# Optimization experiments

Hardware: AMD Instinct MI355X
Metric: run time of the kernel (lower is better)

The kernel has to match this reference:

```python
import jax, jax.numpy as jnp
import numpy as np

DIM = 2048
N_HEADS = 16
Q_LORA = 1536
KV_LORA = 512
NOPE = 128
ROPE = 64
QK_D = NOPE + ROPE  # 192
V_D = 128
EPS = 1e-6
B, S = 2, 2048


def rmsnorm(x, w, eps=EPS):
    return x * jax.lax.rsqrt(jnp.mean(x * x, axis=-1, keepdims=True) + eps) * w


def rotate_pe(x, cos, sin):
    # x: [B, S, H, ROPE]; cos/sin: [S, ROPE] -> broadcast [1, S, 1, ROPE]
    c = cos[None, :, None, :]
    s = sin[None, :, None, :]
    x1, x2 = jnp.split(x, 2, axis=-1)
    rot = jnp.concatenate([-x2, x1], axis=-1)
    return x * c + rot * s


def setup_inputs() -> dict:
    key = jax.random.key(0)
    ks = jax.random.split(key, 8)
    std = 0.02
    x = jax.random.normal(ks[0], (B, S, DIM), dtype=jnp.float32)
    # proper rotary tables
    inv_freq = 1.0 / (10000.0 ** (np.arange(0, ROPE, 2, dtype=np.float32) / ROPE))
    t = np.arange(S, dtype=np.float32)
    freqs = np.outer(t, inv_freq)  # [S, ROPE/2]
    emb = np.concatenate([freqs, freqs], axis=-1)  # [S, ROPE]
    cos = jnp.asarray(np.cos(emb))
    sin = jnp.asarray(np.sin(emb))
    wq_a = jax.random.normal(ks[1], (Q_LORA, DIM), dtype=jnp.float32) * std
    q_norm_w = jnp.ones((Q_LORA,), dtype=jnp.float32)
    wq_b = jax.random.normal(ks[2], (N_HEADS * QK_D, Q_LORA), dtype=jnp.float32) * std
    wkv_a = jax.random.normal(ks[3], (KV_LORA + ROPE, DIM), dtype=jnp.float32) * std
    kv_norm_w = jnp.ones((KV_LORA,), dtype=jnp.float32)
    wkv_b = jax.random.normal(ks[4], (N_HEADS * (NOPE + V_D), KV_LORA), dtype=jnp.float32) * std
    wo = jax.random.normal(ks[5], (DIM, N_HEADS * V_D), dtype=jnp.float32) * std
    return {"x": x, "cos": cos, "sin": sin, "wq_a": wq_a, "q_norm_w": q_norm_w,
            "wq_b": wq_b, "wkv_a": wkv_a, "kv_norm_w": kv_norm_w, "wkv_b": wkv_b, "wo": wo}


def mla_forward(x, cos, sin, wq_a, q_norm_w, wq_b, wkv_a, kv_norm_w, wkv_b, wo):
    bsz, seqlen, _ = x.shape
    scale = QK_D ** (-0.5)
    # Q path: low-rank down-proj -> RMSNorm -> up-proj
    q = rmsnorm(x @ wq_a.T, q_norm_w) @ wq_b.T
    q = q.reshape(bsz, seqlen, N_HEADS, QK_D)
    q_nope, q_pe = q[..., :NOPE], q[..., NOPE:]
    q_pe = rotate_pe(q_pe, cos, sin)
    q = jnp.concatenate([q_nope, q_pe], axis=-1)
    # KV path: shared low-rank latent + single rope slice
    kv = x @ wkv_a.T  # [B, S, KV_LORA + ROPE]
    kv_c, k_pe = kv[..., :KV_LORA], kv[..., KV_LORA:]
    k_pe = rotate_pe(k_pe[:, :, None, :], cos, sin)  # [B, S, 1, ROPE]
    kvb = rmsnorm(kv_c, kv_norm_w) @ wkv_b.T
    kvb = kvb.reshape(bsz, seqlen, N_HEADS, NOPE + V_D)
    k_nope, v = kvb[..., :NOPE], kvb[..., NOPE:]
    k = jnp.concatenate([k_nope, jnp.broadcast_to(k_pe, (bsz, seqlen, N_HEADS, ROPE))], axis=-1)
    # causal attention
    scores = jnp.einsum('bqhd,bkhd->bhqk', q, k) * scale
    mask = jnp.tril(jnp.ones((seqlen, seqlen), dtype=bool))
    scores = jnp.where(mask[None, None], scores, jnp.finfo(scores.dtype).min)
    p = jax.nn.softmax(scores, axis=-1)
    out = jnp.einsum('bhqk,bkhd->bqhd', p, v)
    out = out.reshape(bsz, seqlen, N_HEADS * V_D)
    return out @ wo.T


def reference(x, cos, sin, wq_a, q_norm_w, wq_b, wkv_a, kv_norm_w, wkv_b, wo):
    return mla_forward(x, cos, sin, wq_a, q_norm_w, wq_b, wkv_a, kv_norm_w, wkv_b, wo)
```

## Files before the change

### kernel.cpp

```cpp
#include <hip/hip_runtime.h>

typedef unsigned short u16;
typedef __attribute__((ext_vector_type(8))) short short8;
typedef __attribute__((ext_vector_type(4))) float floatx4;

__device__ __forceinline__ float bf2f(u16 u) {
  union { unsigned int i; float f; } v; v.i = ((unsigned int)u) << 16; return v.f;
}
__device__ __forceinline__ u16 f2bf(float f) {
  union { float f; unsigned int i; } v; v.f = f;
  unsigned int u = v.i;
  u += 0x7fffu + ((u >> 16) & 1u);
  return (u16)(u >> 16);
}

__device__ __forceinline__ void gld_lds16(const void* g, void* l) {
  __builtin_amdgcn_global_load_lds(
      (const __attribute__((address_space(1))) unsigned int*)g,
      (__attribute__((address_space(3))) unsigned int*)l, 16, 0, 0);
}

__global__ __launch_bounds__(256) void f2b_k(const float* __restrict__ s,
                                             u16* __restrict__ d, long n) {
  long i = ((long)blockIdx.x * 256 + threadIdx.x) * 4;
  if (i + 3 < n) {
    float4 v = *(const float4*)(s + i);
    d[i + 0] = f2bf(v.x); d[i + 1] = f2bf(v.y);
    d[i + 2] = f2bf(v.z); d[i + 3] = f2bf(v.w);
  } else {
    for (; i < n; i++) d[i] = f2bf(s[i]);
  }
}

__global__ __launch_bounds__(256) void wcat_k(const float* __restrict__ s1, int r1,
                                              const float* __restrict__ s2, int r2,
                                              u16* __restrict__ d, int cols, int rows_dst) {
  long i = (long)blockIdx.x * 256 + threadIdx.x;
  long total = (long)rows_dst * cols;
  if (i < total) {
    long r = i / cols, c = i - r * cols;
    float v = 0.f;
    if (r < r1) v = s1[r * cols + c];
    else if (r < r1 + r2) v = s2[(r - r1) * cols + c];
    d[i] = f2bf(v);
  }
}

template <int OUT_F32>
__global__ __launch_bounds__(256) void gemm_bt_mfma(
    const u16* __restrict__ A, int lda,
    const u16* __restrict__ W, int ldw,
    void* __restrict__ Cv, int ldc, int K) {
  __shared__ u16 Asm[128 * 32];
  __shared__ u16 Bsm[128 * 32];
  int tid = threadIdx.x;
  int lane = tid & 63, w = tid >> 6;
  int wm = (w >> 1) * 64, wn = (w & 1) * 64;
  int bm = blockIdx.y * 128, bn = blockIdx.x * 128;

  floatx4 acc[4][4];
#pragma unroll
  for (int i = 0; i < 4; i++)
#pragma unroll
    for (int j = 0; j < 4; j++) acc[i][j] = (floatx4){0.f, 0.f, 0.f, 0.f};

  int sr = lane >> 2;
  int sc = (lane & 3) * 8;
  int fr = lane & 15;
  int fq = (lane >> 4) * 8;

  for (int k0 = 0; k0 < K; k0 += 32) {
#pragma unroll
    for (int c = 0; c < 2; c++) {
      int row = 32 * w + 16 * c + sr;
      gld_lds16(A + (size_t)(bm + row) * lda + k0 + sc, &Asm[(32 * w + 16 * c) * 32]);
      gld_lds16(W + (size_t)(bn + row) * ldw + k0 + sc, &Bsm[(32 * w + 16 * c) * 32]);
    }
    __syncthreads();
    short8 af[4], bfr[4];
#pragma unroll
    for (int i = 0; i < 4; i++)
      af[i] = *(const short8*)&Asm[(wm + i * 16 + fr) * 32 + fq];
#pragma unroll
    for (int j = 0; j < 4; j++)
      bfr[j] = *(const short8*)&Bsm[(wn + j * 16 + fr) * 32 + fq];
#pragma unroll
    for (int i = 0; i < 4; i++)
#pragma unroll
      for (int j = 0; j < 4; j++)
        acc[i][j] = __builtin_amdgcn_mfma_f32_16x16x32_bf16(af[i], bfr[j], acc[i][j], 0, 0, 0);
    __syncthreads();
  }

  int cr = (lane >> 4) * 4, cc = lane & 15;
#pragma unroll
  for (int i = 0; i < 4; i++)
#pragma unroll
    for (int j = 0; j < 4; j++) {
      int col = bn + wn + j * 16 + cc;
#pragma unroll
      for (int r = 0; r < 4; r++) {
        size_t row = (size_t)(bm + wm + i * 16 + cr + r);
        if (OUT_F32) ((float*)Cv)[row * ldc + col] = acc[i][j][r];
        else         ((u16*)Cv)[row * ldc + col] = f2bf(acc[i][j][r]);
      }
    }
}

__global__ __launch_bounds__(256) void rmsnorm_k(
    const u16* __restrict__ in, const float* __restrict__ w,
    u16* __restrict__ out, int width, int stride) {
  int row = blockIdx.x;
  const u16* p = in + (size_t)row * stride;
  u16* o = out + (size_t)row * stride;
  float ss = 0.f;
  for (int i = threadIdx.x; i < width; i += 256) { float v = bf2f(p[i]); ss += v * v; }
  for (int off = 32; off > 0; off >>= 1) ss += __shfl_down(ss, off);
  __shared__ float red[4];
  if ((threadIdx.x & 63) == 0) red[threadIdx.x >> 6] = ss;
  __syncthreads();
  float inv = rsqrtf((red[0] + red[1] + red[2] + red[3]) / (float)width + 1e-6f);
  for (int i = threadIdx.x; i < width; i += 256)
    o[i] = f2bf(bf2f(p[i]) * inv * w[i]);
}

__global__ void rope_k(u16* __restrict__ base, int row_stride, int head_stride,
                       int head_off, const float* __restrict__ cosb,
                       const float* __restrict__ sinb, int S) {
  int t = blockIdx.x, h = blockIdx.y, i = threadIdx.x;
  int pos = t % S;
  u16* p = base + (size_t)t * row_stride + h * head_stride + head_off;
  float c1 = cosb[pos * 64 + i];
  float c2 = cosb[pos * 64 + i + 32];
  float s1 = sinb[pos * 64 + i];
  float s2 = sinb[pos * 64 + i + 32];
  float x1 = bf2f(p[i]), x2 = bf2f(p[i + 32]);
  p[i]      = f2bf(x1 * c1 - x2 * s1);
  p[i + 32] = f2bf(x2 * c2 + x1 * s2);
}

__global__ __launch_bounds__(256) void vtrans_k(
    const u16* __restrict__ kvb, u16* __restrict__ vt, int S) {
  int tb = blockIdx.x, h = blockIdx.y, b = blockIdx.z;
  __shared__ __align__(16) u16 Ts[64][136];
  int tid = threadIdx.x;
#pragma unroll
  for (int it = 0; it < 4; it++) {
    int e = tid + 256 * it;
    int tok = e >> 4, c = e & 15;
    short8 v = *(const short8*)(kvb + (size_t)(b * S + tb * 64 + tok) * 4096 + h * 256 + 128 + c * 8);
    *(short8*)&Ts[tok][c * 8] = v;
  }
  __syncthreads();
  int vd = tid >> 1, half = (tid & 1) * 32;
  u16 tmp[32];
#pragma unroll
  for (int j = 0; j < 32; j++) tmp[j] = Ts[half + j][vd];
  u16* dst = vt + ((size_t)((b * 16 + h) * 128) + vd) * S + tb * 64 + half;
#pragma unroll
  for (int c = 0; c < 4; c++)
    *(short8*)(dst + c * 8) = *(short8*)&tmp[c * 8];
}

#define AT_BK 64
__global__ __launch_bounds__(256) void attn_mfma(
    const u16* __restrict__ qf, const u16* __restrict__ kvb,
    const u16* __restrict__ kpe, int kpe_stride, const u16* __restrict__ vt,
    u16* __restrict__ at, int S) {
  int pair = blockIdx.x, h = blockIdx.y, b = blockIdx.z;
  int NT = S / AT_BK;
  int tid = threadIdx.x, lane = tid & 63, w = tid >> 6;
  int fr = lane & 15, fq = lane >> 4;
  int fs = fr & 7;

  __shared__ __align__(16) u16 Ksn[AT_BK * 128];
  __shared__ __align__(16) u16 Ksp[AT_BK * 64];
  __shared__ __align__(16) u16 Vts[128 * AT_BK];
  __shared__ __align__(16) u16 Ps[64 * AT_BK];

  const float scale = 0.07216878364870323f;

  for (int p = 0; p < 2; p++) {
    int qt = p ? (NT - 1 - pair) : pair;
    int q0 = qt * 64;

    short8 qfrag[6];
    {
      const u16* qrow = qf + (size_t)(b * S + q0 + w * 16 + fr) * 3072 + h * 192 + fq * 8;
#pragma unroll
      for (int ks = 0; ks < 6; ks++) qfrag[ks] = *(const short8*)(qrow + ks * 32);
    }

    floatx4 acc_o[8];
#pragma unroll
    for (int j = 0; j < 8; j++) acc_o[j] = (floatx4){0.f, 0.f, 0.f, 0.f};
    float m_r[4], l_r[4];
#pragma unroll
    for (int r = 0; r < 4; r++) { m_r[r] = -3e38f; l_r[r] = 0.f; }

    for (int kt = 0; kt <= qt; kt++) {
      int k0 = kt * AT_BK;
      size_t tokbase = (size_t)(b * S + k0);
#pragma unroll
      for (int c = 0; c < 4; c++) {
        int row = w * 16 + c * 4 + (lane >> 4);
        int cg = (lane & 15) ^ (row & 7);
        gld_lds16(kvb + (tokbase + row) * 4096 + h * 256 + cg * 8,
                  &Ksn[(w * 16 + c * 4) * 128]);
      }
#pragma unroll
      for (int c = 0; c < 2; c++) {
        int row = w * 16 + c * 8 + (lane >> 3);
        int cg = (lane & 7) ^ (row & 7);
        gld_lds16(kpe + (tokbase + row) * kpe_stride + cg * 8,
                  &Ksp[(w * 16 + c * 8) * 64]);
      }
#pragma unroll
      for (int c = 0; c < 4; c++) {
        int vd = w * 32 + c * 8 + (lane >> 3);
        int cg = (lane & 7) ^ (vd & 7);
        gld_lds16(vt + ((size_t)((b * 16 + h) * 128) + vd) * S + k0 + cg * 8,
                  &Vts[(w * 32 + c * 8) * 64]);
      }
      __syncthreads();

      floatx4 accs[4];
#pragma unroll
      for (int nt = 0; nt < 4; nt++) accs[nt] = (floatx4){0.f, 0.f, 0.f, 0.f};
#pragma unroll
      for (int nt = 0; nt < 4; nt++) {
#pragma unroll
        for (int ks = 0; ks < 4; ks++) {
          short8 bf = *(const short8*)&Ksn[(nt * 16 + fr) * 128 + ((ks * 4 + fq) ^ fs) * 8];
          accs[nt] = __builtin_amdgcn_mfma_f32_16x16x32_bf16(qfrag[ks], bf, accs[nt], 0, 0, 0);
        }
#pragma unroll
        for (int ks = 0; ks < 2; ks++) {
          short8 bf = *(const short8*)&Ksp[(nt * 16 + fr) * 64 + ((ks * 4 + fq) ^ fs) * 8];
          accs[nt] = __builtin_amdgcn_mfma_f32_16x16x32_bf16(qfrag[4 + ks], bf, accs[nt], 0, 0, 0);
        }
      }

      bool diag = (kt == qt);
#pragma unroll
      for (int nt = 0; nt < 4; nt++)
#pragma unroll
        for (int r = 0; r < 4; r++) {
          float s = accs[nt][r] * scale;
          if (diag) {
            int col = nt * 16 + fr;
            int row = fq * 4 + r;
            if (k0 + col > q0 + w * 16 + row) s = -3e38f;
          }
          accs[nt][r] = s;
        }

      float alpha[4], rsum[4];
#pragma unroll
      for (int r = 0; r < 4; r++) {
        float mx = fmaxf(fmaxf(accs[0][r], accs[1][r]), fmaxf(accs[2][r], accs[3][r]));
        mx = fmaxf(mx, __shfl_xor(mx, 1));
        mx = fmaxf(mx, __shfl_xor(mx, 2));
        mx = fmaxf(mx, __shfl_xor(mx, 4));
        mx = fmaxf(mx, __shfl_xor(mx, 8));
        float mnew = fmaxf(m_r[r], mx);
        alpha[r] = __expf(m_r[r] - mnew);
        m_r[r] = mnew;
        rsum[r] = 0.f;
      }
#pragma unroll
      for (int nt = 0; nt < 4; nt++)
#pragma unroll
        for (int r = 0; r < 4; r++) {
          float pv = __expf(accs[nt][r] - m_r[r]);
          rsum[r] += pv;
          int row_p = w * 16 + fq * 4 + r;
          int col = nt * 16 + fr;
          Ps[row_p * 64 + (((col >> 3) ^ (row_p & 7)) * 8) + (col & 7)] = f2bf(pv);
        }
#pragma unroll
      for (int r = 0; r < 4; r++) {
        float sm = rsum[r];
        sm += __shfl_xor(sm, 1);
        sm += __shfl_xor(sm, 2);
        sm += __shfl_xor(sm, 4);
        sm += __shfl_xor(sm, 8);
        l_r[r] = l_r[r] * alpha[r] + sm;
      }
      __syncthreads();

#pragma unroll
      for (int j = 0; j < 8; j++)
#pragma unroll
        for (int r = 0; r < 4; r++) acc_o[j][r] *= alpha[r];
      short8 pf0 = *(const short8*)&Ps[(w * 16 + fr) * 64 + (fq ^ fs) * 8];
      short8 pf1 = *(const short8*)&Ps[(w * 16 + fr) * 64 + ((4 + fq) ^ fs) * 8];
#pragma unroll
      for (int j = 0; j < 8; j++) {
        short8 v0 = *(const short8*)&Vts[(j * 16 + fr) * 64 + (fq ^ fs) * 8];
        short8 v1 = *(const short8*)&Vts[(j * 16 + fr) * 64 + ((4 + fq) ^ fs) * 8];
        acc_o[j] = __builtin_amdgcn_mfma_f32_16x16x32_bf16(pf0, v0, acc_o[j], 0, 0, 0);
        acc_o[j] = __builtin_amdgcn_mfma_f32_16x16x32_bf16(pf1, v1, acc_o[j], 0, 0, 0);
      }
      __syncthreads();
    }

    float inv_l[4];
#pragma unroll
    for (int r = 0; r < 4; r++) inv_l[r] = 1.f / l_r[r];
#pragma unroll
    for (int j = 0; j < 8; j++)
#pragma unroll
      for (int r = 0; r < 4; r++) {
        size_t row = (size_t)(b * S + q0 + w * 16 + fq * 4 + r);
        at[row * 2048 + h * 128 + j * 16 + fr] = f2bf(acc_o[j][r] * inv_l[r]);
      }
  }
}

extern "C" void kernel_launch(void* const* d_in, const int* in_sizes, int n_in,
                              void* d_out, int out_size, void* d_ws, size_t ws_size,
                              hipStream_t stream) {
  (void)in_sizes; (void)n_in; (void)out_size; (void)ws_size;
  const float* x     = (const float*)d_in[0];
  const float* cosb  = (const float*)d_in[1];
  const float* sinb  = (const float*)d_in[2];
  const float* wq_a  = (const float*)d_in[3];
  const float* qnw   = (const float*)d_in[4];
  const float* wq_b  = (const float*)d_in[5];
  const float* wkv_a = (const float*)d_in[6];
  const float* kvnw  = (const float*)d_in[7];
  const float* wkv_b = (const float*)d_in[8];
  const float* wo    = (const float*)d_in[9];
  float* out = (float*)d_out;
  const int B = 2, S = 2048, T = B * S;

  char* wsb = (char*)d_ws;
  size_t off = 0;
  u16* xb   = (u16*)(wsb + off); off += (size_t)T * 2048 * 2;
  u16* wcat = (u16*)(wsb + off); off += (size_t)2176 * 2048 * 2;
  u16* wqbb = (u16*)(wsb + off); off += (size_t)3072 * 1536 * 2;
  u16* wkbb = (u16*)(wsb + off); off += (size_t)4096 * 512 * 2;
  u16* wob  = (u16*)(wsb + off); off += (size_t)2048 * 2048 * 2;
  u16* qkv  = (u16*)(wsb + off); off += (size_t)T * 2176 * 2;
  u16* qf   = (u16*)(wsb + off); off += (size_t)T * 3072 * 2;
  u16* kvb  = (u16*)(wsb + off); off += (size_t)T * 4096 * 2;
  u16* at   = (u16*)(wsb + off); off += (size_t)T * 2048 * 2;
  u16* vt   = xb;

  auto conv = [&](const float* s, u16* d, long n) {
    f2b_k<<<(int)((n / 4 + 255) / 256), 256, 0, stream>>>(s, d, n);
  };
  conv(x, xb, (long)T * 2048);
  wcat_k<<<(int)(((long)2176 * 2048 + 255) / 256), 256, 0, stream>>>(
      wq_a, 1536, wkv_a, 576, wcat, 2048, 2176);
  conv(wq_b, wqbb, (long)3072 * 1536);
  conv(wkv_b, wkbb, (long)4096 * 512);
  conv(wo, wob, (long)2048 * 2048);

  gemm_bt_mfma<0><<<dim3(2176 / 128, T / 128), 256, 0, stream>>>(xb, 2048, wcat, 2048, qkv, 2176, 2048);
  rmsnorm_k<<<T, 256, 0, stream>>>(qkv, qnw, qkv, 1536, 2176);
  rmsnorm_k<<<T, 256, 0, stream>>>(qkv + 1536, kvnw, qkv + 1536, 512, 2176);
  rope_k<<<dim3(T, 1), 32, 0, stream>>>(qkv, 2176, 0, 2048, cosb, sinb, S);
  gemm_bt_mfma<0><<<dim3(3072 / 128, T / 128), 256, 0, stream>>>(qkv, 2176, wqbb, 1536, qf, 3072, 1536);
  rope_k<<<dim3(T, 16), 32, 0, stream>>>(qf, 3072, 192, 128, cosb, sinb, S);
  gemm_bt_mfma<0><<<dim3(4096 / 128, T / 128), 256, 0, stream>>>(qkv + 1536, 2176, wkbb, 512, kvb, 4096, 512);
  vtrans_k<<<dim3(S / 64, 16, B), 256, 0, stream>>>(kvb, vt, S);
  attn_mfma<<<dim3(S / 128, 16, B), 256, 0, stream>>>(qf, kvb, qkv + 2048, 2176, vt, at, S);
  gemm_bt_mfma<1><<<dim3(2048 / 128, T / 128), 256, 0, stream>>>(at, 2048, wob, 2048, out, 2048, 2048);
}
```

Measured before the change: 516.9 us.

## Fuse repack, norm+rope, dual GEMMs, and defer softmax row-sum reduction

Merges the five fp32->bf16 conversion launches into one 2D-grid kernel. Fuses both RMSNorms with the k_pe rope into a single per-row kernel. Runs the q up-projection and kv up-projection GEMMs together in one launch so their tiles share the GPU. Attention now uses a flattened grid ordered with heads/batches innermost, and keeps per-lane partial row sums with a single cross-lane reduction at the end instead of every tile. The aim is to cut launch overhead and underfilled small grids, at the cost of a more complex dispatch and an idle kernel-wide grid slot for the padded repack regions.

```diff
diff --git a/kernel.cpp b/kernel.cpp
--- a/kernel.cpp
+++ b/kernel.cpp
@@ -20,30 +20,92 @@
       (__attribute__((address_space(3))) unsigned int*)l, 16, 0, 0);
 }
 
-__global__ __launch_bounds__(256) void f2b_k(const float* __restrict__ s,
-                                             u16* __restrict__ d, long n) {
+__global__ __launch_bounds__(256) void repack_all_k(
+    const float* __restrict__ x, const float* __restrict__ wqa,
+    const float* __restrict__ wkva, const float* __restrict__ wqb,
+    const float* __restrict__ wkvb, const float* __restrict__ wo,
+    u16* __restrict__ xb, u16* __restrict__ wcat, u16* __restrict__ wqbb,
+    u16* __restrict__ wkbb, u16* __restrict__ wob) {
   long i = ((long)blockIdx.x * 256 + threadIdx.x) * 4;
-  if (i + 3 < n) {
-    float4 v = *(const float4*)(s + i);
-    d[i + 0] = f2bf(v.x); d[i + 1] = f2bf(v.y);
-    d[i + 2] = f2bf(v.z); d[i + 3] = f2bf(v.w);
+  int region = blockIdx.y;
+  const float* s = nullptr; u16* d = nullptr; long n = 0;
+  switch (region) {
+    case 0: s = x;    d = xb;   n = 4096L * 2048; break;
+    case 1: s = nullptr; d = wcat; n = 2176L * 2048; break;
+    case 2: s = wqb;  d = wqbb; n = 3072L * 1536; break;
+    case 3: s = wkvb; d = wkbb; n = 4096L * 512;  break;
+    case 4: s = wo;   d = wob;  n = 2048L * 2048; break;
+  }
+  if (i >= n) return;
+  float4 v;
+  if (region == 1) {
+    long r = i >> 11, c = i & 2047;
+    if (r < 1536)      v = *(const float4*)(wqa + r * 2048 + c);
+    else if (r < 2112) v = *(const float4*)(wkva + (r - 1536) * 2048 + c);
+    else               v = (float4){0.f, 0.f, 0.f, 0.f};
   } else {
-    for (; i < n; i++) d[i] = f2bf(s[i]);
-  }
-}
-
-__global__ __launch_bounds__(256) void wcat_k(const float* __restrict__ s1, int r1,
-                                              const float* __restrict__ s2, int r2,
-                                              u16* __restrict__ d, int cols, int rows_dst) {
-  long i = (long)blockIdx.x * 256 + threadIdx.x;
-  long total = (long)rows_dst * cols;
-  if (i < total) {
-    long r = i / cols, c = i - r * cols;
-    float v = 0.f;
-    if (r < r1) v = s1[r * cols + c];
-    else if (r < r1 + r2) v = s2[(r - r1) * cols + c];
-    d[i] = f2bf(v);
-  }
+    v = *(const float4*)(s + i);
+  }
+  d[i + 0] = f2bf(v.x); d[i + 1] = f2bf(v.y);
+  d[i + 2] = f2bf(v.z); d[i + 3] = f2bf(v.w);
+}
+
+template <int OUT_F32>
+__device__ __forceinline__ void gemm_tile(
+    const u16* __restrict__ A, int lda, const u16* __restrict__ W, int ldw,
+    void* __restrict__ Cv, int ldc, int K, int bm, int bn,
+    u16* Asm, u16* Bsm) {
+  int tid = threadIdx.x;
+  int lane = tid & 63, w = tid >> 6;
+  int wm = (w >> 1) * 64, wn = (w & 1) * 64;
+
+  floatx4 acc[4][4];
+#pragma unroll
+  for (int i = 0; i < 4; i++)
+#pragma unroll
+    for (int j = 0; j < 4; j++) acc[i][j] = (floatx4){0.f, 0.f, 0.f, 0.f};
+
+  int sr = lane >> 2;
+  int sc = (lane & 3) * 8;
+  int fr = lane & 15;
+  int fq = (lane >> 4) * 8;
+
+  for (int k0 = 0; k0 < K; k0 += 32) {
+#pragma unroll
+    for (int c = 0; c < 2; c++) {
+      int row = 32 * w + 16 * c + sr;
+      gld_lds16(A + (size_t)(bm + row) * lda + k0 + sc, &Asm[(32 * w + 16 * c) * 32]);
+      gld_lds16(W + (size_t)(bn + row) * ldw + k0 + sc, &Bsm[(32 * w + 16 * c) * 32]);
+    }
+    __syncthreads();
+    short8 af[4], bfr[4];
+#pragma unroll
+    for (int i = 0; i < 4; i++)
+      af[i] = *(const short8*)&Asm[(wm + i * 16 + fr) * 32 + fq];
+#pragma unroll
+    for (int j = 0; j < 4; j++)
+      bfr[j] = *(const short8*)&Bsm[(wn + j * 16 + fr) * 32 + fq];
+#pragma unroll
+    for (int i = 0; i < 4; i++)
+#pragma unroll
+      for (int j = 0; j < 4; j++)
+        acc[i][j] = __builtin_amdgcn_mfma_f32_16x16x32_bf16(af[i], bfr[j], acc[i][j], 0, 0, 0);
+    __syncthreads();
+  }
+
+  int cr = (lane >> 4) * 4, cc = lane & 15;
+#pragma unroll
+  for (int i = 0; i < 4; i++)
+#pragma unroll
+    for (int j = 0; j < 4; j++) {
+      int col = bn + wn + j * 16 + cc;
+#pragma unroll
+      for (int r = 0; r < 4; r++) {
+        size_t row = (size_t)(bm + wm + i * 16 + cr + r);
+        if (OUT_F32) ((float*)Cv)[row * ldc + col] = acc[i][j][r];
+        else         ((u16*)Cv)[row * ldc + col] = f2bf(acc[i][j][r]);
+      }
+    }
 }
 
 template <int OUT_F32>
@@ -53,75 +115,63 @@
     void* __restrict__ Cv, int ldc, int K) {
   __shared__ u16 Asm[128 * 32];
   __shared__ u16 Bsm[128 * 32];
-  int tid = threadIdx.x;
-  int lane = tid & 63, w = tid >> 6;
-  int wm = (w >> 1) * 64, wn = (w & 1) * 64;
-  int bm = blockIdx.y * 128, bn = blockIdx.x * 128;
-
-  floatx4 acc[4][4];
-#pragma unroll
-  for (int i = 0; i < 4; i++)
-#pragma unroll
-    for (int j = 0; j < 4; j++) acc[i][j] = (floatx4){0.f, 0.f, 0.f, 0.f};
-
-  int sr = lane >> 2;
-  int sc = (lane & 3) * 8;
-  int fr = lane & 15;
-  int fq = (lane >> 4) * 8;
-
-  for (int k0 = 0; k0 < K; k0 += 32) {
-#pragma unroll
-    for (int c = 0; c < 2; c++) {
-      int row = 32 * w + 16 * c + sr;
-      gld_lds16(A + (size_t)(bm + row) * lda + k0 + sc, &Asm[(32 * w + 16 * c) * 32]);
-      gld_lds16(W + (size_t)(bn + row) * ldw + k0 + sc, &Bsm[(32 * w + 16 * c) * 32]);
-    }
-    __syncthreads();
-    short8 af[4], bfr[4];
-#pragma unroll
-    for (int i = 0; i < 4; i++)
-      af[i] = *(const short8*)&Asm[(wm + i * 16 + fr) * 32 + fq];
-#pragma unroll
-    for (int j = 0; j < 4; j++)
-      bfr[j] = *(const short8*)&Bsm[(wn + j * 16 + fr) * 32 + fq];
-#pragma unroll
-    for (int i = 0; i < 4; i++)
-#pragma unroll
-      for (int j = 0; j < 4; j++)
-        acc[i][j] = __builtin_amdgcn_mfma_f32_16x16x32_bf16(af[i], bfr[j], acc[i][j], 0, 0, 0);
-    __syncthreads();
-  }
-
-  int cr = (lane >> 4) * 4, cc = lane & 15;
-#pragma unroll
-  for (int i = 0; i < 4; i++)
-#pragma unroll
-    for (int j = 0; j < 4; j++) {
-      int col = bn + wn + j * 16 + cc;
-#pragma unroll
-      for (int r = 0; r < 4; r++) {
-        size_t row = (size_t)(bm + wm + i * 16 + cr + r);
-        if (OUT_F32) ((float*)Cv)[row * ldc + col] = acc[i][j][r];
-        else         ((u16*)Cv)[row * ldc + col] = f2bf(acc[i][j][r]);
-      }
-    }
-}
-
-__global__ __launch_bounds__(256) void rmsnorm_k(
-    const u16* __restrict__ in, const float* __restrict__ w,
-    u16* __restrict__ out, int width, int stride) {
-  int row = blockIdx.x;
-  const u16* p = in + (size_t)row * stride;
-  u16* o = out + (size_t)row * stride;
-  float ss = 0.f;
-  for (int i = threadIdx.x; i < width; i += 256) { float v = bf2f(p[i]); ss += v * v; }
-  for (int off = 32; off > 0; off >>= 1) ss += __shfl_down(ss, off);
-  __shared__ float red[4];
-  if ((threadIdx.x & 63) == 0) red[threadIdx.x >> 6] = ss;
+  gemm_tile<OUT_F32>(A, lda, W, ldw, Cv, ldc, K, blockIdx.y * 128, blockIdx.x * 128, Asm, Bsm);
+}
+
+__global__ __launch_bounds__(256) void gemm_dual_mfma(
+    const u16* __restrict__ A1, int lda1, const u16* __restrict__ W1, int ldw1,
+    u16* __restrict__ C1, int ldc1, int K1, int nt1,
+    const u16* __restrict__ A2, int lda2, const u16* __restrict__ W2, int ldw2,
+    u16* __restrict__ C2, int ldc2, int K2) {
+  __shared__ u16 Asm[128 * 32];
+  __shared__ u16 Bsm[128 * 32];
+  int bx = blockIdx.x;
+  if (bx < nt1)
+    gemm_tile<0>(A1, lda1, W1, ldw1, C1, ldc1, K1, blockIdx.y * 128, bx * 128, Asm, Bsm);
+  else
+    gemm_tile<0>(A2, lda2, W2, ldw2, C2, ldc2, K2, blockIdx.y * 128, (bx - nt1) * 128, Asm, Bsm);
+}
+
+__global__ __launch_bounds__(256) void normrope_k(
+    u16* __restrict__ qkv, const float* __restrict__ qnw,
+    const float* __restrict__ kvnw, const float* __restrict__ cosb,
+    const float* __restrict__ sinb, int S) {
+  int row = blockIdx.x, tid = threadIdx.x;
+  u16* p = qkv + (size_t)row * 2176;
+  float s1 = 0.f, s2 = 0.f;
+#pragma unroll
+  for (int it = 0; it < 6; it++) { float v = bf2f(p[tid + 256 * it]); s1 += v * v; }
+#pragma unroll
+  for (int it = 0; it < 2; it++) { float v = bf2f(p[1536 + tid + 256 * it]); s2 += v * v; }
+  for (int off = 32; off > 0; off >>= 1) {
+    s1 += __shfl_down(s1, off);
+    s2 += __shfl_down(s2, off);
+  }
+  __shared__ float red1[4], red2[4];
+  if ((tid & 63) == 0) { red1[tid >> 6] = s1; red2[tid >> 6] = s2; }
   __syncthreads();
-  float inv = rsqrtf((red[0] + red[1] + red[2] + red[3]) / (float)width + 1e-6f);
-  for (int i = threadIdx.x; i < width; i += 256)
-    o[i] = f2bf(bf2f(p[i]) * inv * w[i]);
+  float inv1 = rsqrtf((red1[0] + red1[1] + red1[2] + red1[3]) / 1536.f + 1e-6f);
+  float inv2 = rsqrtf((red2[0] + red2[1] + red2[2] + red2[3]) / 512.f + 1e-6f);
+#pragma unroll
+  for (int it = 0; it < 6; it++) {
+    int i = tid + 256 * it;
+    p[i] = f2bf(bf2f(p[i]) * inv1 * qnw[i]);
+  }
+#pragma unroll
+  for (int it = 0; it < 2; it++) {
+    int i = tid + 256 * it;
+    p[1536 + i] = f2bf(bf2f(p[1536 + i]) * inv2 * kvnw[i]);
+  }
+  if (tid < 32) {
+    int pos = row % S;
+    float c1 = cosb[pos * 64 + tid];
+    float c2 = cosb[pos * 64 + tid + 32];
+    float sn1 = sinb[pos * 64 + tid];
+    float sn2 = sinb[pos * 64 + tid + 32];
+    float x1 = bf2f(p[2048 + tid]), x2 = bf2f(p[2048 + tid + 32]);
+    p[2048 + tid]      = f2bf(x1 * c1 - x2 * sn1);
+    p[2048 + tid + 32] = f2bf(x2 * c2 + x1 * sn2);
+  }
 }
 
 __global__ void rope_k(u16* __restrict__ base, int row_stride, int head_stride,
@@ -167,7 +217,9 @@
     const u16* __restrict__ qf, const u16* __restrict__ kvb,
     const u16* __restrict__ kpe, int kpe_stride, const u16* __restrict__ vt,
     u16* __restrict__ at, int S) {
-  int pair = blockIdx.x, h = blockIdx.y, b = blockIdx.z;
+  int id = blockIdx.x;
+  int pair = id >> 5, hb = id & 31;
+  int h = hb & 15, b = hb >> 4;
   int NT = S / AT_BK;
   int tid = threadIdx.x, lane = tid & 63, w = tid >> 6;
   int fr = lane & 15, fq = lane >> 4;
@@ -255,7 +307,7 @@
           accs[nt][r] = s;
         }
 
-      float alpha[4], rsum[4];
+      float alpha[4];
 #pragma unroll
       for (int r = 0; r < 4; r++) {
         float mx = fmaxf(fmaxf(accs[0][r], accs[1][r]), fmaxf(accs[2][r], accs[3][r]));
@@ -266,27 +318,18 @@
         float mnew = fmaxf(m_r[r], mx);
         alpha[r] = __expf(m_r[r] - mnew);
         m_r[r] = mnew;
-        rsum[r] = 0.f;
+        l_r[r] *= alpha[r];
       }
 #pragma unroll
       for (int nt = 0; nt < 4; nt++)
 #pragma unroll
         for (int r = 0; r < 4; r++) {
           float pv = __expf(accs[nt][r] - m_r[r]);
-          rsum[r] += pv;
+          l_r[r] += pv;
           int row_p = w * 16 + fq * 4 + r;
           int col = nt * 16 + fr;
           Ps[row_p * 64 + (((col >> 3) ^ (row_p & 7)) * 8) + (col & 7)] = f2bf(pv);
         }
-#pragma unroll
-      for (int r = 0; r < 4; r++) {
-        float sm = rsum[r];
-        sm += __shfl_xor(sm, 1);
-        sm += __shfl_xor(sm, 2);
-        sm += __shfl_xor(sm, 4);
-        sm += __shfl_xor(sm, 8);
-        l_r[r] = l_r[r] * alpha[r] + sm;
-      }
       __syncthreads();
 
 #pragma unroll
@@ -307,7 +350,14 @@
 
     float inv_l[4];
 #pragma unroll
-    for (int r = 0; r < 4; r++) inv_l[r] = 1.f / l_r[r];
+    for (int r = 0; r < 4; r++) {
+      float sm = l_r[r];
+      sm += __shfl_xor(sm, 1);
+      sm += __shfl_xor(sm, 2);
+      sm += __shfl_xor(sm, 4);
+      sm += __shfl_xor(sm, 8);
+      inv_l[r] = 1.f / sm;
+    }
 #pragma unroll
     for (int j = 0; j < 8; j++)
 #pragma unroll
@@ -348,24 +398,16 @@
   u16* at   = (u16*)(wsb + off); off += (size_t)T * 2048 * 2;
   u16* vt   = xb;
 
-  auto conv = [&](const float* s, u16* d, long n) {
-    f2b_k<<<(int)((n / 4 + 255) / 256), 256, 0, stream>>>(s, d, n);
-  };
-  conv(x, xb, (long)T * 2048);
-  wcat_k<<<(int)(((long)2176 * 2048 + 255) / 256), 256, 0, stream>>>(
-      wq_a, 1536, wkv_a, 576, wcat, 2048, 2176);
-  conv(wq_b, wqbb, (long)3072 * 1536);
-  conv(wkv_b, wkbb, (long)4096 * 512);
-  conv(wo, wob, (long)2048 * 2048);
+  repack_all_k<<<dim3(8192, 5), 256, 0, stream>>>(
+      x, wq_a, wkv_a, wq_b, wkv_b, wo, xb, wcat, wqbb, wkbb, wob);
 
   gemm_bt_mfma<0><<<dim3(2176 / 128, T / 128), 256, 0, stream>>>(xb, 2048, wcat, 2048, qkv, 2176, 2048);
-  rmsnorm_k<<<T, 256, 0, stream>>>(qkv, qnw, qkv, 1536, 2176);
-  rmsnorm_k<<<T, 256, 0, stream>>>(qkv + 1536, kvnw, qkv + 1536, 512, 2176);
-  rope_k<<<dim3(T, 1), 32, 0, stream>>>(qkv, 2176, 0, 2048, cosb, sinb, S);
-  gemm_bt_mfma<0><<<dim3(3072 / 128, T / 128), 256, 0, stream>>>(qkv, 2176, wqbb, 1536, qf, 3072, 1536);
+  normrope_k<<<T, 256, 0, stream>>>(qkv, qnw, kvnw, cosb, sinb, S);
+  gemm_dual_mfma<<<dim3(3072 / 128 + 4096 / 128, T / 128), 256, 0, stream>>>(
+      qkv, 2176, wqbb, 1536, qf, 3072, 1536, 3072 / 128,
+      qkv + 1536, 2176, wkbb, 512, kvb, 4096, 512);
   rope_k<<<dim3(T, 16), 32, 0, stream>>>(qf, 3072, 192, 128, cosb, sinb, S);
-  gemm_bt_mfma<0><<<dim3(4096 / 128, T / 128), 256, 0, stream>>>(qkv + 1536, 2176, wkbb, 512, kvb, 4096, 512);
   vtrans_k<<<dim3(S / 64, 16, B), 256, 0, stream>>>(kvb, vt, S);
-  attn_mfma<<<dim3(S / 128, 16, B), 256, 0, stream>>>(qf, kvb, qkv + 2048, 2176, vt, at, S);
+  attn_mfma<<<dim3((S / 128) * 32), 256, 0, stream>>>(qf, kvb, qkv + 2048, 2176, vt, at, S);
   gemm_bt_mfma<1><<<dim3(2048 / 128, T / 128), 256, 0, stream>>>(at, 2048, wob, 2048, out, 2048, 2048);
 }
```

Result: faster. 481.4 us (-6.9%).
